# Kernel optimization log

Hardware: AMD Instinct MI355X
Metric: run time of the kernel (lower is better)

The kernel has to match this reference:

```python
import jax, jax.numpy as jnp
import numpy as np

N, E = 50000, 800000
IN_DIM, HID, OUT, HEADS = 128, 128, 64, 4
C1 = HID // HEADS  # 32 per-head channels in gat1
NEG_SLOPE = 0.2


def _gat_conv(x, src, dst, W, a_src, a_dst, b, heads, ch):
    """PyG GATConv (inference): gather -> edge attention -> segment softmax -> scatter."""
    n = x.shape[0]
    h = (x @ W).reshape(n, heads, ch)                      # [N,H,C]
    alpha_src = jnp.einsum('nhc,hc->nh', h, a_src)         # [N,H]
    alpha_dst = jnp.einsum('nhc,hc->nh', h, a_dst)         # [N,H]
    e = jax.nn.leaky_relu(alpha_src[src] + alpha_dst[dst], NEG_SLOPE)  # [E,H]
    m = jax.ops.segment_max(e, dst, num_segments=n)        # per-target max (stable softmax)
    e = jnp.exp(e - m[dst])
    denom = jax.ops.segment_sum(e, dst, num_segments=n)
    alpha = e / (denom[dst] + 1e-16)                       # [E,H]
    out = jax.ops.segment_sum(h[src] * alpha[:, :, None], dst, num_segments=n)  # [N,H,C]
    return out.reshape(n, heads * ch) + b


def setup_inputs() -> dict:
    key = jax.random.key(0)
    ks = jax.random.split(key, 16)
    x = jax.random.normal(ks[0], (N, IN_DIM), dtype=jnp.float32)
    edge_index = jax.random.randint(ks[1], (2, E), 0, N, dtype=jnp.int64)
    s = lambda fan_in: 1.0 / np.sqrt(fan_in)
    return {
        'x': x,
        'edge_index': edge_index,
        'W1': jax.random.normal(ks[2], (IN_DIM, HEADS * C1), jnp.float32) * s(IN_DIM),
        'a_src1': jax.random.normal(ks[3], (HEADS, C1), jnp.float32) * s(C1),
        'a_dst1': jax.random.normal(ks[4], (HEADS, C1), jnp.float32) * s(C1),
        'b1': jnp.zeros((HID,), jnp.float32),
        'W2': jax.random.normal(ks[5], (HID, OUT), jnp.float32) * s(HID),
        'a_src2': jax.random.normal(ks[6], (1, OUT), jnp.float32) * s(OUT),
        'a_dst2': jax.random.normal(ks[7], (1, OUT), jnp.float32) * s(OUT),
        'b2': jnp.zeros((OUT,), jnp.float32),
        'pw1': jax.random.normal(ks[8], (OUT, OUT), jnp.float32) * s(OUT),
        'pb1': jnp.zeros((OUT,), jnp.float32),
        'pw2': jax.random.normal(ks[9], (OUT, OUT), jnp.float32) * s(OUT),
        'pb2': jnp.zeros((OUT,), jnp.float32),
    }


def reference(x, edge_index, W1, a_src1, a_dst1, b1, W2, a_src2, a_dst2, b2, pw1, pb1, pw2, pb2):
    n = x.shape[0]
    # PyG GATConv add_self_loops=True
    loops = jnp.arange(n, dtype=edge_index.dtype)
    src = jnp.concatenate([edge_index[0], loops])
    dst = jnp.concatenate([edge_index[1], loops])
    h = jax.nn.elu(_gat_conv(x, src, dst, W1, a_src1, a_dst1, b1, HEADS, C1))
    h = jax.nn.elu(_gat_conv(h, src, dst, W2, a_src2, a_dst2, b2, 1, OUT))
    # origin_proj: Linear -> ReLU -> Linear
    h = jax.nn.relu(h @ pw1 + pb1)
    return h @ pw2 + pb2
```

## Files before the change

kernel.cpp:

```cpp
#include <hip/hip_runtime.h>
#include <math.h>

#define N_NODES 50000
#define N_EDGES 800000
#define ET (N_EDGES + N_NODES)
#define IN_DIM 128
#define HID 128
#define OUT_DIM 64
#define BW 64
#define NBUCK ((N_NODES + BW - 1) / BW)
#define NBLK 256
#define EPB 3328

typedef __attribute__((ext_vector_type(8))) short bf16x8;
typedef __attribute__((ext_vector_type(4))) float f32x4;

__device__ __forceinline__ float lrelu(float x){ return x >= 0.f ? x : 0.2f * x; }
__device__ __forceinline__ float eluf(float x){ return x > 0.f ? x : expm1f(x); }
__device__ __forceinline__ unsigned f2bf(float f){
    unsigned u = __float_as_uint(f);
    return (u + 0x7fffu + ((u >> 16) & 1u)) >> 16;
}
__device__ __forceinline__ float bflo(unsigned u){ return __uint_as_float(u << 16); }
__device__ __forceinline__ float bfhi(unsigned u){ return __uint_as_float(u & 0xffff0000u); }

__global__ __launch_bounds__(256) void k_count(const int* __restrict__ dst, int* __restrict__ C)
{
    __shared__ int cnt[NBUCK];
    const int tid = threadIdx.x, blk = blockIdx.x;
    for (int i = tid; i < NBUCK; i += 256) cnt[i] = 0;
    __syncthreads();
    #pragma unroll
    for (int j = 0; j < EPB / 256; j++) {
        const int e = blk * EPB + j * 256 + tid;
        if (e < ET) {
            const int d = (e < N_EDGES) ? dst[e] : (e - N_EDGES);
            atomicAdd(&cnt[d >> 6], 1);
        }
    }
    __syncthreads();
    for (int b = tid; b < NBUCK; b += 256) C[b * NBLK + blk] = cnt[b];
}

__global__ __launch_bounds__(256) void k_bsumA(const int* __restrict__ C, int* __restrict__ bsum2)
{
    __shared__ int red[4];
    int v = C[blockIdx.x * NBLK + threadIdx.x];
    #pragma unroll
    for (int off = 32; off > 0; off >>= 1) v += __shfl_down(v, off);
    if ((threadIdx.x & 63) == 0) red[threadIdx.x >> 6] = v;
    __syncthreads();
    if (threadIdx.x == 0) bsum2[blockIdx.x] = red[0] + red[1] + red[2] + red[3];
}

__global__ __launch_bounds__(1024) void k_bscanB(const int* __restrict__ bsum2, int* __restrict__ boff2)
{
    __shared__ int part[1024];
    const int t = threadIdx.x;
    int v = (t < NBUCK) ? bsum2[t] : 0;
    part[t] = v;
    __syncthreads();
    #pragma unroll
    for (int d = 1; d < 1024; d <<= 1) {
        int add = (t >= d) ? part[t - d] : 0;
        __syncthreads();
        part[t] += add;
        __syncthreads();
    }
    if (t < NBUCK) boff2[t] = part[t] - v;
    if (t == 0) boff2[NBUCK] = ET;
}

__global__ __launch_bounds__(256) void k_cscanC(const int* __restrict__ C,
                                                const int* __restrict__ boff2,
                                                int* __restrict__ Cs)
{
    __shared__ int part[256];
    const int t = threadIdx.x, b = blockIdx.x;
    int v = C[b * NBLK + t];
    part[t] = v;
    __syncthreads();
    #pragma unroll
    for (int d = 1; d < 256; d <<= 1) {
        int add = (t >= d) ? part[t - d] : 0;
        __syncthreads();
        part[t] += add;
        __syncthreads();
    }
    Cs[b * NBLK + t] = boff2[b] + part[t] - v;
}

__global__ __launch_bounds__(256) void k_part2(const int* __restrict__ src,
                                               const int* __restrict__ dst,
                                               const int* __restrict__ Cs,
                                               uint2* __restrict__ part)
{
    __shared__ int base[NBUCK];
    __shared__ int cnt[NBUCK];
    const int tid = threadIdx.x, blk = blockIdx.x;
    for (int b = tid; b < NBUCK; b += 256) { base[b] = Cs[b * NBLK + blk]; cnt[b] = 0; }
    __syncthreads();
    #pragma unroll
    for (int j = 0; j < EPB / 256; j++) {
        const int e = blk * EPB + j * 256 + tid;
        if (e < ET) {
            int s, d;
            if (e < N_EDGES) { s = src[e]; d = dst[e]; } else { s = d = e - N_EDGES; }
            const int b = d >> 6;
            const int r = atomicAdd(&cnt[b], 1);
            part[base[b] + r] = make_uint2((unsigned)d, (unsigned)s);
        }
    }
}

__global__ __launch_bounds__(256) void k_scat2(const int* __restrict__ boff2,
                                               const uint2* __restrict__ part,
                                               int* __restrict__ rowptr,
                                               int* __restrict__ csr_src)
{
    __shared__ int cnt64[BW];
    __shared__ int nbase[BW];
    const int b = blockIdx.x, tid = threadIdx.x;
    const int n0 = b * BW;
    const int lo = boff2[b], hi = boff2[b + 1];
    if (tid < BW) cnt64[tid] = 0;
    __syncthreads();
    for (int i = lo + tid; i < hi; i += 256) {
        atomicAdd(&cnt64[part[i].x & (BW - 1)], 1);
    }
    __syncthreads();
    if (tid < BW) {
        int v = cnt64[tid];
        int incl = v;
        #pragma unroll
        for (int off = 1; off < 64; off <<= 1) {
            int t2 = __shfl_up(incl, off);
            if (tid >= off) incl += t2;
        }
        const int excl = incl - v;
        nbase[tid] = excl;
        const int n = n0 + tid;
        if (n < N_NODES) rowptr[n] = lo + excl;
        cnt64[tid] = 0;
    }
    if (b == 0 && tid == 0) rowptr[N_NODES] = ET;
    __syncthreads();
    for (int i = lo + tid; i < hi; i += 256) {
        const uint2 p = part[i];
        const int dn = (int)p.x & (BW - 1);
        const int r = atomicAdd(&cnt64[dn], 1);
        csr_src[lo + nbase[dn] + r] = (int)p.y;
    }
}

__global__ __launch_bounds__(256, 2) void k_gemm1(
    const float* __restrict__ x, const float* __restrict__ W1,
    const float* __restrict__ a_s, const float* __restrict__ a_d,
    unsigned* __restrict__ h1b, float* __restrict__ as1, float* __restrict__ ad1)
{
    __shared__ unsigned sWt[128 * 68];
    __shared__ unsigned sxb[64 * 68];
    const int tid = threadIdx.x;
    const int wave = tid >> 6;
    const int lane = tid & 63;
    const int ll   = lane & 15;
    const int quad = lane >> 4;
    const int n0 = blockIdx.x * 64;

    for (int idx = tid; idx < 8192; idx += 256) {
        const int n = idx & 127, kp = idx >> 7;
        const float w0 = W1[(2 * kp) * 128 + n];
        const float w1 = W1[(2 * kp + 1) * 128 + n];
        sWt[n * 68 + kp] = f2bf(w0) | (f2bf(w1) << 16);
    }
    for (int idx = tid; idx < 4096; idx += 256) {
        const int node = idx >> 6, kp = idx & 63;
        const int n = n0 + node;
        unsigned pk = 0;
        if (n < N_NODES) {
            const float x0 = x[n * 128 + 2 * kp];
            const float x1 = x[n * 128 + 2 * kp + 1];
            pk = f2bf(x0) | (f2bf(x1) << 16);
        }
        sxb[node * 68 + kp] = pk;
    }
    __syncthreads();

    f32x4 acc[8];
    #pragma unroll
    for (int t = 0; t < 8; t++) acc[t] = (f32x4){0.f, 0.f, 0.f, 0.f};

    #pragma unroll
    for (int kk = 0; kk < 4; kk++) {
        const int kpo = 16 * kk + 4 * quad;
        const bf16x8 a = *(const bf16x8*)&sxb[(16 * wave + ll) * 68 + kpo];
        #pragma unroll
        for (int t = 0; t < 8; t++) {
            const bf16x8 b = *(const bf16x8*)&sWt[(16 * t + ll) * 68 + kpo];
            acc[t] = __builtin_amdgcn_mfma_f32_16x16x32_bf16(a, b, acc[t], 0, 0, 0);
        }
    }

    float as_v[8], ad_v[8];
    #pragma unroll
    for (int t = 0; t < 8; t++) { as_v[t] = a_s[16 * t + ll]; ad_v[t] = a_d[16 * t + ll]; }
    unsigned short* h1u = (unsigned short*)h1b;
    #pragma unroll
    for (int r = 0; r < 4; r++) {
        const int n = n0 + 16 * wave + 4 * quad + r;
        float ps0 = acc[0][r] * as_v[0] + acc[1][r] * as_v[1];
        float ps1 = acc[2][r] * as_v[2] + acc[3][r] * as_v[3];
        float ps2 = acc[4][r] * as_v[4] + acc[5][r] * as_v[5];
        float ps3 = acc[6][r] * as_v[6] + acc[7][r] * as_v[7];
        float pd0 = acc[0][r] * ad_v[0] + acc[1][r] * ad_v[1];
        float pd1 = acc[2][r] * ad_v[2] + acc[3][r] * ad_v[3];
        float pd2 = acc[4][r] * ad_v[4] + acc[5][r] * ad_v[5];
        float pd3 = acc[6][r] * ad_v[6] + acc[7][r] * ad_v[7];
        #pragma unroll
        for (int off = 1; off < 16; off <<= 1) {
            ps0 += __shfl_xor(ps0, off); ps1 += __shfl_xor(ps1, off);
            ps2 += __shfl_xor(ps2, off); ps3 += __shfl_xor(ps3, off);
            pd0 += __shfl_xor(pd0, off); pd1 += __shfl_xor(pd1, off);
            pd2 += __shfl_xor(pd2, off); pd3 += __shfl_xor(pd3, off);
        }
        if (n < N_NODES) {
            #pragma unroll
            for (int t = 0; t < 8; t++)
                h1u[n * 128 + 16 * t + ll] = (unsigned short)f2bf(acc[t][r]);
            if (ll == 0) {
                as1[n * 4 + 0] = ps0; as1[n * 4 + 1] = ps1;
                as1[n * 4 + 2] = ps2; as1[n * 4 + 3] = ps3;
                ad1[n * 4 + 0] = pd0; ad1[n * 4 + 1] = pd1;
                ad1[n * 4 + 2] = pd2; ad1[n * 4 + 3] = pd3;
            }
        }
    }
}

__global__ __launch_bounds__(256) void k_aggr1(
    const int* __restrict__ rowptr, const int* __restrict__ csr_src,
    const float* __restrict__ as1, const float* __restrict__ ad1,
    const uint4* __restrict__ h1u4, float* __restrict__ acc1)
{
    const int d  = blockIdx.x * 16 + (threadIdx.x >> 4);
    const int c8 = threadIdx.x & 15;
    const int hd = c8 >> 2;
    const int r0 = rowptr[d], r1 = rowptr[d + 1];
    const float adv = ad1[d * 4 + hd];
    float den = 0.f;
    float acc[8];
    #pragma unroll
    for (int m = 0; m < 8; m++) acc[m] = 0.f;
    int i = r0;
    for (; i + 2 <= r1; i += 2) {
        const int s0 = csr_src[i], s1 = csr_src[i + 1];
        const float e0 = as1[s0 * 4 + hd], e1 = as1[s1 * 4 + hd];
        const uint4 u0 = h1u4[s0 * 16 + c8];
        const uint4 u1 = h1u4[s1 * 16 + c8];
        const float w0 = expf(lrelu(e0 + adv));
        const float w1 = expf(lrelu(e1 + adv));
        den += w0 + w1;
        acc[0] = fmaf(bflo(u0.x), w0, acc[0]); acc[1] = fmaf(bfhi(u0.x), w0, acc[1]);
        acc[2] = fmaf(bflo(u0.y), w0, acc[2]); acc[3] = fmaf(bfhi(u0.y), w0, acc[3]);
        acc[4] = fmaf(bflo(u0.z), w0, acc[4]); acc[5] = fmaf(bfhi(u0.z), w0, acc[5]);
        acc[6] = fmaf(bflo(u0.w), w0, acc[6]); acc[7] = fmaf(bfhi(u0.w), w0, acc[7]);
        acc[0] = fmaf(bflo(u1.x), w1, acc[0]); acc[1] = fmaf(bfhi(u1.x), w1, acc[1]);
        acc[2] = fmaf(bflo(u1.y), w1, acc[2]); acc[3] = fmaf(bfhi(u1.y), w1, acc[3]);
        acc[4] = fmaf(bflo(u1.z), w1, acc[4]); acc[5] = fmaf(bfhi(u1.z), w1, acc[5]);
        acc[6] = fmaf(bflo(u1.w), w1, acc[6]); acc[7] = fmaf(bfhi(u1.w), w1, acc[7]);
    }
    if (i < r1) {
        const int s = csr_src[i];
        const float w = expf(lrelu(as1[s * 4 + hd] + adv));
        const uint4 u = h1u4[s * 16 + c8];
        den += w;
        acc[0] = fmaf(bflo(u.x), w, acc[0]); acc[1] = fmaf(bfhi(u.x), w, acc[1]);
        acc[2] = fmaf(bflo(u.y), w, acc[2]); acc[3] = fmaf(bfhi(u.y), w, acc[3]);
        acc[4] = fmaf(bflo(u.z), w, acc[4]); acc[5] = fmaf(bfhi(u.z), w, acc[5]);
        acc[6] = fmaf(bflo(u.w), w, acc[6]); acc[7] = fmaf(bfhi(u.w), w, acc[7]);
    }
    const float inv = 1.f / (den + 1e-16f);
    float4 o0 = make_float4(acc[0] * inv, acc[1] * inv, acc[2] * inv, acc[3] * inv);
    float4 o1 = make_float4(acc[4] * inv, acc[5] * inv, acc[6] * inv, acc[7] * inv);
    ((float4*)acc1)[d * 32 + 2 * c8 + 0] = o0;
    ((float4*)acc1)[d * 32 + 2 * c8 + 1] = o1;
}

__global__ __launch_bounds__(256, 4) void k_layer2(
    const float* __restrict__ acc1, const float* __restrict__ b1,
    const float* __restrict__ W2, const float* __restrict__ a_s2, const float* __restrict__ a_d2,
    unsigned* __restrict__ h2b, float* __restrict__ as2, float* __restrict__ ad2)
{
    __shared__ unsigned sWt[64 * 68];
    __shared__ unsigned sxb[64 * 68];
    const int tid = threadIdx.x;
    const int wave = tid >> 6;
    const int lane = tid & 63;
    const int ll   = lane & 15;
    const int quad = lane >> 4;
    const int n0 = blockIdx.x * 64;

    for (int idx = tid; idx < 4096; idx += 256) {
        const int n = idx & 63, kp = idx >> 6;
        const float w0 = W2[(2 * kp) * 64 + n];
        const float w1 = W2[(2 * kp + 1) * 64 + n];
        sWt[n * 68 + kp] = f2bf(w0) | (f2bf(w1) << 16);
    }
    for (int idx = tid; idx < 4096; idx += 256) {
        const int node = idx >> 6, kp = idx & 63;
        const int n = n0 + node;
        unsigned pk = 0;
        if (n < N_NODES) {
            const float v0 = eluf(acc1[n * 128 + 2 * kp]     + b1[2 * kp]);
            const float v1 = eluf(acc1[n * 128 + 2 * kp + 1] + b1[2 * kp + 1]);
            pk = f2bf(v0) | (f2bf(v1) << 16);
        }
        sxb[node * 68 + kp] = pk;
    }
    __syncthreads();

    f32x4 acc[4];
    #pragma unroll
    for (int t = 0; t < 4; t++) acc[t] = (f32x4){0.f, 0.f, 0.f, 0.f};

    #pragma unroll
    for (int kk = 0; kk < 4; kk++) {
        const int kpo = 16 * kk + 4 * quad;
        const bf16x8 a = *(const bf16x8*)&sxb[(16 * wave + ll) * 68 + kpo];
        #pragma unroll
        for (int t = 0; t < 4; t++) {
            const bf16x8 b = *(const bf16x8*)&sWt[(16 * t + ll) * 68 + kpo];
            acc[t] = __builtin_amdgcn_mfma_f32_16x16x32_bf16(a, b, acc[t], 0, 0, 0);
        }
    }

    float as_v[4], ad_v[4];
    #pragma unroll
    for (int t = 0; t < 4; t++) { as_v[t] = a_s2[16 * t + ll]; ad_v[t] = a_d2[16 * t + ll]; }
    unsigned short* h2u = (unsigned short*)h2b;
    #pragma unroll
    for (int r = 0; r < 4; r++) {
        const int n = n0 + 16 * wave + 4 * quad + r;
        float ps = acc[0][r] * as_v[0] + acc[1][r] * as_v[1]
                 + acc[2][r] * as_v[2] + acc[3][r] * as_v[3];
        float pd = acc[0][r] * ad_v[0] + acc[1][r] * ad_v[1]
                 + acc[2][r] * ad_v[2] + acc[3][r] * ad_v[3];
        #pragma unroll
        for (int off = 1; off < 16; off <<= 1) {
            ps += __shfl_xor(ps, off);
            pd += __shfl_xor(pd, off);
        }
        if (n < N_NODES) {
            #pragma unroll
            for (int t = 0; t < 4; t++)
                h2u[n * 64 + 16 * t + ll] = (unsigned short)f2bf(acc[t][r]);
            if (ll == 0) { as2[n] = ps; ad2[n] = pd; }
        }
    }
}

__global__ __launch_bounds__(256) void k_aggr2(
    const int* __restrict__ rowptr, const int* __restrict__ csr_src,
    const float* __restrict__ as2, const float* __restrict__ ad2,
    const uint4* __restrict__ h2u4, float* __restrict__ acc2)
{
    const int d  = blockIdx.x * 32 + (threadIdx.x >> 3);
    const int c8 = threadIdx.x & 7;
    if (d >= N_NODES) return;
    const int r0 = rowptr[d], r1 = rowptr[d + 1];
    const float adv = ad2[d];
    float den = 0.f;
    float acc[8];
    #pragma unroll
    for (int m = 0; m < 8; m++) acc[m] = 0.f;
    int i = r0;
    for (; i + 2 <= r1; i += 2) {
        const int s0 = csr_src[i], s1 = csr_src[i + 1];
        const float e0 = as2[s0], e1 = as2[s1];
        const uint4 u0 = h2u4[s0 * 8 + c8];
        const uint4 u1 = h2u4[s1 * 8 + c8];
        const float w0 = expf(lrelu(e0 + adv));
        const float w1 = expf(lrelu(e1 + adv));
        den += w0 + w1;
        acc[0] = fmaf(bflo(u0.x), w0, acc[0]); acc[1] = fmaf(bfhi(u0.x), w0, acc[1]);
        acc[2] = fmaf(bflo(u0.y), w0, acc[2]); acc[3] = fmaf(bfhi(u0.y), w0, acc[3]);
        acc[4] = fmaf(bflo(u0.z), w0, acc[4]); acc[5] = fmaf(bfhi(u0.z), w0, acc[5]);
        acc[6] = fmaf(bflo(u0.w), w0, acc[6]); acc[7] = fmaf(bfhi(u0.w), w0, acc[7]);
        acc[0] = fmaf(bflo(u1.x), w1, acc[0]); acc[1] = fmaf(bfhi(u1.x), w1, acc[1]);
        acc[2] = fmaf(bflo(u1.y), w1, acc[2]); acc[3] = fmaf(bfhi(u1.y), w1, acc[3]);
        acc[4] = fmaf(bflo(u1.z), w1, acc[4]); acc[5] = fmaf(bfhi(u1.z), w1, acc[5]);
        acc[6] = fmaf(bflo(u1.w), w1, acc[6]); acc[7] = fmaf(bfhi(u1.w), w1, acc[7]);
    }
    if (i < r1) {
        const int s = csr_src[i];
        const float w = expf(lrelu(as2[s] + adv));
        const uint4 u = h2u4[s * 8 + c8];
        den += w;
        acc[0] = fmaf(bflo(u.x), w, acc[0]); acc[1] = fmaf(bfhi(u.x), w, acc[1]);
        acc[2] = fmaf(bflo(u.y), w, acc[2]); acc[3] = fmaf(bfhi(u.y), w, acc[3]);
        acc[4] = fmaf(bflo(u.z), w, acc[4]); acc[5] = fmaf(bfhi(u.z), w, acc[5]);
        acc[6] = fmaf(bflo(u.w), w, acc[6]); acc[7] = fmaf(bfhi(u.w), w, acc[7]);
    }
    const float inv = 1.f / (den + 1e-16f);
    float4 o0 = make_float4(acc[0] * inv, acc[1] * inv, acc[2] * inv, acc[3] * inv);
    float4 o1 = make_float4(acc[4] * inv, acc[5] * inv, acc[6] * inv, acc[7] * inv);
    ((float4*)acc2)[d * 16 + 2 * c8 + 0] = o0;
    ((float4*)acc2)[d * 16 + 2 * c8 + 1] = o1;
}

__global__ __launch_bounds__(256, 2) void k_out(
    const float* __restrict__ acc2, const float* __restrict__ b2,
    const float* __restrict__ pw1, const float* __restrict__ pb1,
    const float* __restrict__ pw2, const float* __restrict__ pb2,
    float* __restrict__ out)
{
    __shared__ float s1[64 * 64];
    __shared__ float s2[64 * 64];
    __shared__ float so[64][68];
    __shared__ float sp[64][68];
    const int tid = threadIdx.x;
    for (int i = tid; i < 1024; i += 256) {
        ((float4*)s1)[i] = ((const float4*)pw1)[i];
        ((float4*)s2)[i] = ((const float4*)pw2)[i];
    }
    const int cg = tid & 15;
    const int ng = tid >> 4;
    const float4 pb1_4 = ((const float4*)pb1)[cg];
    const float4 pb2_4 = ((const float4*)pb2)[cg];
    const int nGroups = (N_NODES + 63) / 64;
    for (int g = blockIdx.x; g < nGroups; g += gridDim.x) {
        const int n0 = g * 64;
        __syncthreads();
        #pragma unroll
        for (int j = 0; j < 4; j++) {
            const int i = tid + 256 * j;
            const int node = i >> 4, quad = i & 15;
            const int n = n0 + node;
            float4 v = make_float4(0.f, 0.f, 0.f, 0.f);
            if (n < N_NODES) {
                v = ((const float4*)acc2)[n * 16 + quad];
                const float4 bb = ((const float4*)b2)[quad];
                v.x = eluf(v.x + bb.x);
                v.y = eluf(v.y + bb.y);
                v.z = eluf(v.z + bb.z);
                v.w = eluf(v.w + bb.w);
            }
            *(float4*)&so[node][4 * quad] = v;
        }
        __syncthreads();
        float4 p[4];
        #pragma unroll
        for (int m = 0; m < 4; m++) p[m] = pb1_4;
        #pragma unroll 8
        for (int k = 0; k < 64; k++) {
            const float4 w = *(const float4*)&s1[k * 64 + 4 * cg];
            #pragma unroll
            for (int m = 0; m < 4; m++) {
                const float xv = so[4 * ng + m][k];
                p[m].x = fmaf(xv, w.x, p[m].x);
                p[m].y = fmaf(xv, w.y, p[m].y);
                p[m].z = fmaf(xv, w.z, p[m].z);
                p[m].w = fmaf(xv, w.w, p[m].w);
            }
        }
        #pragma unroll
        for (int m = 0; m < 4; m++) {
            p[m].x = fmaxf(p[m].x, 0.f); p[m].y = fmaxf(p[m].y, 0.f);
            p[m].z = fmaxf(p[m].z, 0.f); p[m].w = fmaxf(p[m].w, 0.f);
            *(float4*)&sp[4 * ng + m][4 * cg] = p[m];
        }
        __syncthreads();
        float4 o[4];
        #pragma unroll
        for (int m = 0; m < 4; m++) o[m] = pb2_4;
        #pragma unroll 8
        for (int k = 0; k < 64; k++) {
            const float4 w = *(const float4*)&s2[k * 64 + 4 * cg];
            #pragma unroll
            for (int m = 0; m < 4; m++) {
                const float xv = sp[4 * ng + m][k];
                o[m].x = fmaf(xv, w.x, o[m].x);
                o[m].y = fmaf(xv, w.y, o[m].y);
                o[m].z = fmaf(xv, w.z, o[m].z);
                o[m].w = fmaf(xv, w.w, o[m].w);
            }
        }
        #pragma unroll
        for (int m = 0; m < 4; m++) {
            const int n = n0 + 4 * ng + m;
            if (n < N_NODES) ((float4*)out)[n * 16 + cg] = o[m];
        }
    }
}

extern "C" void kernel_launch(void* const* d_in, const int* in_sizes, int n_in,
                              void* d_out, int out_size, void* d_ws, size_t ws_size,
                              hipStream_t stream)
{
    const float* x      = (const float*)d_in[0];
    const int*   ei     = (const int*)d_in[1];
    const int*   src    = ei;
    const int*   dst    = ei + N_EDGES;
    const float* W1     = (const float*)d_in[2];
    const float* a_src1 = (const float*)d_in[3];
    const float* a_dst1 = (const float*)d_in[4];
    const float* b1     = (const float*)d_in[5];
    const float* W2     = (const float*)d_in[6];
    const float* a_src2 = (const float*)d_in[7];
    const float* a_dst2 = (const float*)d_in[8];
    const float* b2     = (const float*)d_in[9];
    const float* pw1    = (const float*)d_in[10];
    const float* pb1    = (const float*)d_in[11];
    const float* pw2    = (const float*)d_in[12];
    const float* pb2    = (const float*)d_in[13];

    uint2* part  = (uint2*)d_ws;
    int* ibase   = (int*)(part + ET);
    int* rowptr  = ibase;
    int* C       = rowptr + 50001;
    int* Cs      = C + 200192;
    int* bsum2   = Cs + 200192;
    int* boff2   = bsum2 + 782;
    int* csr_src = boff2 + 785;
    unsigned* h1b = (unsigned*)(csr_src + 850000);
    unsigned* h2b = h1b + 3200000;
    float* fws   = (float*)(h2b + 1600000);
    float* as1   = fws;
    float* ad1   = as1 + 200000;
    float* acc1  = ad1 + 200000;
    float* as2   = acc1 + 6400000;
    float* ad2   = as2 + 50000;
    float* acc2  = ad2 + 50000;

    k_count<<<NBLK, 256, 0, stream>>>(dst, C);
    k_bsumA<<<NBUCK, 256, 0, stream>>>(C, bsum2);
    k_bscanB<<<1, 1024, 0, stream>>>(bsum2, boff2);
    k_cscanC<<<NBUCK, 256, 0, stream>>>(C, boff2, Cs);
    k_part2<<<NBLK, 256, 0, stream>>>(src, dst, Cs, part);
    k_scat2<<<NBUCK, 256, 0, stream>>>(boff2, part, rowptr, csr_src);

    k_gemm1<<<(N_NODES + 63) / 64, 256, 0, stream>>>(x, W1, a_src1, a_dst1, h1b, as1, ad1);
    k_aggr1<<<N_NODES / 16, 256, 0, stream>>>(rowptr, csr_src, as1, ad1,
                                              (const uint4*)h1b, acc1);

    k_layer2<<<(N_NODES + 63) / 64, 256, 0, stream>>>(acc1, b1, W2, a_src2, a_dst2, h2b, as2, ad2);
    k_aggr2<<<(N_NODES + 31) / 32, 256, 0, stream>>>(rowptr, csr_src, as2, ad2,
                                                     (const uint4*)h2b, acc2);

    k_out<<<782, 256, 0, stream>>>(acc2, b2, pw1, pb1, pw2, pb2, (float*)d_out);
}
```

Before: 249.0 us.

## Fuse gemm1 with partition, fold bias+ELU into aggr1, merge aggr2 with output MLP

Merges the layer-1 GEMM and the edge partition kernel into one launch with block-index dispatch so the two independent jobs run concurrently. Layer-1 aggregation now applies bias and ELU and writes bf16 directly, so layer 2 loads half as much data and the fp32 intermediate goes away. Layer-2 aggregation is fused with the two-layer output MLP in a 512-thread kernel, removing the acc2 round trip. Both aggregation loops are unrolled by four to keep more gathers in flight, at the cost of more register pressure.

```diff
diff --git a/kernel.cpp b/kernel.cpp
--- a/kernel.cpp
+++ b/kernel.cpp
@@ -11,6 +11,7 @@
 #define NBUCK ((N_NODES + BW - 1) / BW)
 #define NBLK 256
 #define EPB 3328
+#define NT64 ((N_NODES + 63) / 64)
 
 typedef __attribute__((ext_vector_type(8))) short bf16x8;
 typedef __attribute__((ext_vector_type(4))) float f32x4;
@@ -90,25 +91,109 @@
     Cs[b * NBLK + t] = boff2[b] + part[t] - v;
 }
 
-__global__ __launch_bounds__(256) void k_part2(const int* __restrict__ src,
-                                               const int* __restrict__ dst,
-                                               const int* __restrict__ Cs,
-                                               uint2* __restrict__ part)
-{
-    __shared__ int base[NBUCK];
-    __shared__ int cnt[NBUCK];
-    const int tid = threadIdx.x, blk = blockIdx.x;
-    for (int b = tid; b < NBUCK; b += 256) { base[b] = Cs[b * NBLK + blk]; cnt[b] = 0; }
-    __syncthreads();
-    #pragma unroll
-    for (int j = 0; j < EPB / 256; j++) {
-        const int e = blk * EPB + j * 256 + tid;
-        if (e < ET) {
-            int s, d;
-            if (e < N_EDGES) { s = src[e]; d = dst[e]; } else { s = d = e - N_EDGES; }
-            const int b = d >> 6;
-            const int r = atomicAdd(&cnt[b], 1);
-            part[base[b] + r] = make_uint2((unsigned)d, (unsigned)s);
+__global__ __launch_bounds__(256, 2) void k_gemm1_part2(
+    const float* __restrict__ x, const float* __restrict__ W1,
+    const float* __restrict__ a_s, const float* __restrict__ a_d,
+    unsigned* __restrict__ h1b, float* __restrict__ as1, float* __restrict__ ad1,
+    const int* __restrict__ src, const int* __restrict__ dst,
+    const int* __restrict__ Cs, uint2* __restrict__ part)
+{
+    __shared__ unsigned smem[128 * 68 + 64 * 68];
+    const int tid = threadIdx.x;
+
+    if (blockIdx.x < NT64) {
+        unsigned* sWt = smem;
+        unsigned* sxb = smem + 128 * 68;
+        const int wave = tid >> 6;
+        const int lane = tid & 63;
+        const int ll   = lane & 15;
+        const int quad = lane >> 4;
+        const int n0 = blockIdx.x * 64;
+
+        for (int idx = tid; idx < 8192; idx += 256) {
+            const int n = idx & 127, kp = idx >> 7;
+            const float w0 = W1[(2 * kp) * 128 + n];
+            const float w1 = W1[(2 * kp + 1) * 128 + n];
+            sWt[n * 68 + kp] = f2bf(w0) | (f2bf(w1) << 16);
+        }
+        for (int idx = tid; idx < 4096; idx += 256) {
+            const int node = idx >> 6, kp = idx & 63;
+            const int n = n0 + node;
+            unsigned pk = 0;
+            if (n < N_NODES) {
+                const float x0 = x[n * 128 + 2 * kp];
+                const float x1 = x[n * 128 + 2 * kp + 1];
+                pk = f2bf(x0) | (f2bf(x1) << 16);
+            }
+            sxb[node * 68 + kp] = pk;
+        }
+        __syncthreads();
+
+        f32x4 acc[8];
+        #pragma unroll
+        for (int t = 0; t < 8; t++) acc[t] = (f32x4){0.f, 0.f, 0.f, 0.f};
+
+        #pragma unroll
+        for (int kk = 0; kk < 4; kk++) {
+            const int kpo = 16 * kk + 4 * quad;
+            const bf16x8 a = *(const bf16x8*)&sxb[(16 * wave + ll) * 68 + kpo];
+            #pragma unroll
+            for (int t = 0; t < 8; t++) {
+                const bf16x8 b = *(const bf16x8*)&sWt[(16 * t + ll) * 68 + kpo];
+                acc[t] = __builtin_amdgcn_mfma_f32_16x16x32_bf16(a, b, acc[t], 0, 0, 0);
+            }
+        }
+
+        float as_v[8], ad_v[8];
+        #pragma unroll
+        for (int t = 0; t < 8; t++) { as_v[t] = a_s[16 * t + ll]; ad_v[t] = a_d[16 * t + ll]; }
+        unsigned short* h1u = (unsigned short*)h1b;
+        #pragma unroll
+        for (int r = 0; r < 4; r++) {
+            const int n = n0 + 16 * wave + 4 * quad + r;
+            float ps0 = acc[0][r] * as_v[0] + acc[1][r] * as_v[1];
+            float ps1 = acc[2][r] * as_v[2] + acc[3][r] * as_v[3];
+            float ps2 = acc[4][r] * as_v[4] + acc[5][r] * as_v[5];
+            float ps3 = acc[6][r] * as_v[6] + acc[7][r] * as_v[7];
+            float pd0 = acc[0][r] * ad_v[0] + acc[1][r] * ad_v[1];
+            float pd1 = acc[2][r] * ad_v[2] + acc[3][r] * ad_v[3];
+            float pd2 = acc[4][r] * ad_v[4] + acc[5][r] * ad_v[5];
+            float pd3 = acc[6][r] * ad_v[6] + acc[7][r] * ad_v[7];
+            #pragma unroll
+            for (int off = 1; off < 16; off <<= 1) {
+                ps0 += __shfl_xor(ps0, off); ps1 += __shfl_xor(ps1, off);
+                ps2 += __shfl_xor(ps2, off); ps3 += __shfl_xor(ps3, off);
+                pd0 += __shfl_xor(pd0, off); pd1 += __shfl_xor(pd1, off);
+                pd2 += __shfl_xor(pd2, off); pd3 += __shfl_xor(pd3, off);
+            }
+            if (n < N_NODES) {
+                #pragma unroll
+                for (int t = 0; t < 8; t++)
+                    h1u[n * 128 + 16 * t + ll] = (unsigned short)f2bf(acc[t][r]);
+                if (ll == 0) {
+                    as1[n * 4 + 0] = ps0; as1[n * 4 + 1] = ps1;
+                    as1[n * 4 + 2] = ps2; as1[n * 4 + 3] = ps3;
+                    ad1[n * 4 + 0] = pd0; ad1[n * 4 + 1] = pd1;
+                    ad1[n * 4 + 2] = pd2; ad1[n * 4 + 3] = pd3;
+                }
+            }
+        }
+    } else {
+        const int blk = blockIdx.x - NT64;
+        int* base = (int*)smem;
+        int* cnt  = (int*)smem + NBUCK;
+        for (int b = tid; b < NBUCK; b += 256) { base[b] = Cs[b * NBLK + blk]; cnt[b] = 0; }
+        __syncthreads();
+        #pragma unroll
+        for (int j = 0; j < EPB / 256; j++) {
+            const int e = blk * EPB + j * 256 + tid;
+            if (e < ET) {
+                int s, d;
+                if (e < N_EDGES) { s = src[e]; d = dst[e]; } else { s = d = e - N_EDGES; }
+                const int b = d >> 6;
+                const int r = atomicAdd(&cnt[b], 1);
+                part[base[b] + r] = make_uint2((unsigned)d, (unsigned)s);
+            }
         }
     }
 }
@@ -153,94 +238,11 @@
     }
 }
 
-__global__ __launch_bounds__(256, 2) void k_gemm1(
-    const float* __restrict__ x, const float* __restrict__ W1,
-    const float* __restrict__ a_s, const float* __restrict__ a_d,
-    unsigned* __restrict__ h1b, float* __restrict__ as1, float* __restrict__ ad1)
-{
-    __shared__ unsigned sWt[128 * 68];
-    __shared__ unsigned sxb[64 * 68];
-    const int tid = threadIdx.x;
-    const int wave = tid >> 6;
-    const int lane = tid & 63;
-    const int ll   = lane & 15;
-    const int quad = lane >> 4;
-    const int n0 = blockIdx.x * 64;
-
-    for (int idx = tid; idx < 8192; idx += 256) {
-        const int n = idx & 127, kp = idx >> 7;
-        const float w0 = W1[(2 * kp) * 128 + n];
-        const float w1 = W1[(2 * kp + 1) * 128 + n];
-        sWt[n * 68 + kp] = f2bf(w0) | (f2bf(w1) << 16);
-    }
-    for (int idx = tid; idx < 4096; idx += 256) {
-        const int node = idx >> 6, kp = idx & 63;
-        const int n = n0 + node;
-        unsigned pk = 0;
-        if (n < N_NODES) {
-            const float x0 = x[n * 128 + 2 * kp];
-            const float x1 = x[n * 128 + 2 * kp + 1];
-            pk = f2bf(x0) | (f2bf(x1) << 16);
-        }
-        sxb[node * 68 + kp] = pk;
-    }
-    __syncthreads();
-
-    f32x4 acc[8];
-    #pragma unroll
-    for (int t = 0; t < 8; t++) acc[t] = (f32x4){0.f, 0.f, 0.f, 0.f};
-
-    #pragma unroll
-    for (int kk = 0; kk < 4; kk++) {
-        const int kpo = 16 * kk + 4 * quad;
-        const bf16x8 a = *(const bf16x8*)&sxb[(16 * wave + ll) * 68 + kpo];
-        #pragma unroll
-        for (int t = 0; t < 8; t++) {
-            const bf16x8 b = *(const bf16x8*)&sWt[(16 * t + ll) * 68 + kpo];
-            acc[t] = __builtin_amdgcn_mfma_f32_16x16x32_bf16(a, b, acc[t], 0, 0, 0);
-        }
-    }
-
-    float as_v[8], ad_v[8];
-    #pragma unroll
-    for (int t = 0; t < 8; t++) { as_v[t] = a_s[16 * t + ll]; ad_v[t] = a_d[16 * t + ll]; }
-    unsigned short* h1u = (unsigned short*)h1b;
-    #pragma unroll
-    for (int r = 0; r < 4; r++) {
-        const int n = n0 + 16 * wave + 4 * quad + r;
-        float ps0 = acc[0][r] * as_v[0] + acc[1][r] * as_v[1];
-        float ps1 = acc[2][r] * as_v[2] + acc[3][r] * as_v[3];
-        float ps2 = acc[4][r] * as_v[4] + acc[5][r] * as_v[5];
-        float ps3 = acc[6][r] * as_v[6] + acc[7][r] * as_v[7];
-        float pd0 = acc[0][r] * ad_v[0] + acc[1][r] * ad_v[1];
-        float pd1 = acc[2][r] * ad_v[2] + acc[3][r] * ad_v[3];
-        float pd2 = acc[4][r] * ad_v[4] + acc[5][r] * ad_v[5];
-        float pd3 = acc[6][r] * ad_v[6] + acc[7][r] * ad_v[7];
-        #pragma unroll
-        for (int off = 1; off < 16; off <<= 1) {
-            ps0 += __shfl_xor(ps0, off); ps1 += __shfl_xor(ps1, off);
-            ps2 += __shfl_xor(ps2, off); ps3 += __shfl_xor(ps3, off);
-            pd0 += __shfl_xor(pd0, off); pd1 += __shfl_xor(pd1, off);
-            pd2 += __shfl_xor(pd2, off); pd3 += __shfl_xor(pd3, off);
-        }
-        if (n < N_NODES) {
-            #pragma unroll
-            for (int t = 0; t < 8; t++)
-                h1u[n * 128 + 16 * t + ll] = (unsigned short)f2bf(acc[t][r]);
-            if (ll == 0) {
-                as1[n * 4 + 0] = ps0; as1[n * 4 + 1] = ps1;
-                as1[n * 4 + 2] = ps2; as1[n * 4 + 3] = ps3;
-                ad1[n * 4 + 0] = pd0; ad1[n * 4 + 1] = pd1;
-                ad1[n * 4 + 2] = pd2; ad1[n * 4 + 3] = pd3;
-            }
-        }
-    }
-}
-
 __global__ __launch_bounds__(256) void k_aggr1(
     const int* __restrict__ rowptr, const int* __restrict__ csr_src,
     const float* __restrict__ as1, const float* __restrict__ ad1,
-    const uint4* __restrict__ h1u4, float* __restrict__ acc1)
+    const uint4* __restrict__ h1u4, const float* __restrict__ b1,
+    unsigned* __restrict__ hEb)
 {
     const int d  = blockIdx.x * 16 + (threadIdx.x >> 4);
     const int c8 = threadIdx.x & 15;
@@ -252,14 +254,20 @@
     #pragma unroll
     for (int m = 0; m < 8; m++) acc[m] = 0.f;
     int i = r0;
-    for (; i + 2 <= r1; i += 2) {
-        const int s0 = csr_src[i], s1 = csr_src[i + 1];
+    for (; i + 4 <= r1; i += 4) {
+        const int s0 = csr_src[i],     s1 = csr_src[i + 1];
+        const int s2 = csr_src[i + 2], s3 = csr_src[i + 3];
         const float e0 = as1[s0 * 4 + hd], e1 = as1[s1 * 4 + hd];
+        const float e2 = as1[s2 * 4 + hd], e3 = as1[s3 * 4 + hd];
         const uint4 u0 = h1u4[s0 * 16 + c8];
         const uint4 u1 = h1u4[s1 * 16 + c8];
+        const uint4 u2 = h1u4[s2 * 16 + c8];
+        const uint4 u3 = h1u4[s3 * 16 + c8];
         const float w0 = expf(lrelu(e0 + adv));
         const float w1 = expf(lrelu(e1 + adv));
-        den += w0 + w1;
+        const float w2 = expf(lrelu(e2 + adv));
+        const float w3 = expf(lrelu(e3 + adv));
+        den += (w0 + w1) + (w2 + w3);
         acc[0] = fmaf(bflo(u0.x), w0, acc[0]); acc[1] = fmaf(bfhi(u0.x), w0, acc[1]);
         acc[2] = fmaf(bflo(u0.y), w0, acc[2]); acc[3] = fmaf(bfhi(u0.y), w0, acc[3]);
         acc[4] = fmaf(bflo(u0.z), w0, acc[4]); acc[5] = fmaf(bfhi(u0.z), w0, acc[5]);
@@ -268,8 +276,16 @@
         acc[2] = fmaf(bflo(u1.y), w1, acc[2]); acc[3] = fmaf(bfhi(u1.y), w1, acc[3]);
         acc[4] = fmaf(bflo(u1.z), w1, acc[4]); acc[5] = fmaf(bfhi(u1.z), w1, acc[5]);
         acc[6] = fmaf(bflo(u1.w), w1, acc[6]); acc[7] = fmaf(bfhi(u1.w), w1, acc[7]);
-    }
-    if (i < r1) {
+        acc[0] = fmaf(bflo(u2.x), w2, acc[0]); acc[1] = fmaf(bfhi(u2.x), w2, acc[1]);
+        acc[2] = fmaf(bflo(u2.y), w2, acc[2]); acc[3] = fmaf(bfhi(u2.y), w2, acc[3]);
+        acc[4] = fmaf(bflo(u2.z), w2, acc[4]); acc[5] = fmaf(bfhi(u2.z), w2, acc[5]);
+        acc[6] = fmaf(bflo(u2.w), w2, acc[6]); acc[7] = fmaf(bfhi(u2.w), w2, acc[7]);
+        acc[0] = fmaf(bflo(u3.x), w3, acc[0]); acc[1] = fmaf(bfhi(u3.x), w3, acc[1]);
+        acc[2] = fmaf(bflo(u3.y), w3, acc[2]); acc[3] = fmaf(bfhi(u3.y), w3, acc[3]);
+        acc[4] = fmaf(bflo(u3.z), w3, acc[4]); acc[5] = fmaf(bfhi(u3.z), w3, acc[5]);
+        acc[6] = fmaf(bflo(u3.w), w3, acc[6]); acc[7] = fmaf(bfhi(u3.w), w3, acc[7]);
+    }
+    for (; i < r1; ++i) {
         const int s = csr_src[i];
         const float w = expf(lrelu(as1[s * 4 + hd] + adv));
         const uint4 u = h1u4[s * 16 + c8];
@@ -280,14 +296,26 @@
         acc[6] = fmaf(bflo(u.w), w, acc[6]); acc[7] = fmaf(bfhi(u.w), w, acc[7]);
     }
     const float inv = 1.f / (den + 1e-16f);
-    float4 o0 = make_float4(acc[0] * inv, acc[1] * inv, acc[2] * inv, acc[3] * inv);
-    float4 o1 = make_float4(acc[4] * inv, acc[5] * inv, acc[6] * inv, acc[7] * inv);
-    ((float4*)acc1)[d * 32 + 2 * c8 + 0] = o0;
-    ((float4*)acc1)[d * 32 + 2 * c8 + 1] = o1;
+    const float4 bA = ((const float4*)b1)[2 * c8];
+    const float4 bB = ((const float4*)b1)[2 * c8 + 1];
+    const float v0 = eluf(acc[0] * inv + bA.x);
+    const float v1 = eluf(acc[1] * inv + bA.y);
+    const float v2 = eluf(acc[2] * inv + bA.z);
+    const float v3 = eluf(acc[3] * inv + bA.w);
+    const float v4 = eluf(acc[4] * inv + bB.x);
+    const float v5 = eluf(acc[5] * inv + bB.y);
+    const float v6 = eluf(acc[6] * inv + bB.z);
+    const float v7 = eluf(acc[7] * inv + bB.w);
+    uint4 o;
+    o.x = f2bf(v0) | (f2bf(v1) << 16);
+    o.y = f2bf(v2) | (f2bf(v3) << 16);
+    o.z = f2bf(v4) | (f2bf(v5) << 16);
+    o.w = f2bf(v6) | (f2bf(v7) << 16);
+    ((uint4*)hEb)[d * 16 + c8] = o;
 }
 
 __global__ __launch_bounds__(256, 4) void k_layer2(
-    const float* __restrict__ acc1, const float* __restrict__ b1,
+    const unsigned* __restrict__ hEb,
     const float* __restrict__ W2, const float* __restrict__ a_s2, const float* __restrict__ a_d2,
     unsigned* __restrict__ h2b, float* __restrict__ as2, float* __restrict__ ad2)
 {
@@ -306,16 +334,14 @@
         const float w1 = W2[(2 * kp + 1) * 64 + n];
         sWt[n * 68 + kp] = f2bf(w0) | (f2bf(w1) << 16);
     }
-    for (int idx = tid; idx < 4096; idx += 256) {
-        const int node = idx >> 6, kp = idx & 63;
+    const uint4* hE4 = (const uint4*)hEb;
+    for (int idx = tid; idx < 1024; idx += 256) {
+        const int node = idx >> 4, q = idx & 15;
         const int n = n0 + node;
-        unsigned pk = 0;
-        if (n < N_NODES) {
-            const float v0 = eluf(acc1[n * 128 + 2 * kp]     + b1[2 * kp]);
-            const float v1 = eluf(acc1[n * 128 + 2 * kp + 1] + b1[2 * kp + 1]);
-            pk = f2bf(v0) | (f2bf(v1) << 16);
-        }
-        sxb[node * 68 + kp] = pk;
+        uint4 pk = make_uint4(0, 0, 0, 0);
+        if (n < N_NODES) pk = hE4[n * 16 + q];
+        unsigned* dstp = &sxb[node * 68 + 4 * q];
+        dstp[0] = pk.x; dstp[1] = pk.y; dstp[2] = pk.z; dstp[3] = pk.w;
     }
     __syncthreads();
 
@@ -359,57 +385,10 @@
     }
 }
 
-__global__ __launch_bounds__(256) void k_aggr2(
+__global__ __launch_bounds__(512, 4) void k_tail(
     const int* __restrict__ rowptr, const int* __restrict__ csr_src,
     const float* __restrict__ as2, const float* __restrict__ ad2,
-    const uint4* __restrict__ h2u4, float* __restrict__ acc2)
-{
-    const int d  = blockIdx.x * 32 + (threadIdx.x >> 3);
-    const int c8 = threadIdx.x & 7;
-    if (d >= N_NODES) return;
-    const int r0 = rowptr[d], r1 = rowptr[d + 1];
-    const float adv = ad2[d];
-    float den = 0.f;
-    float acc[8];
-    #pragma unroll
-    for (int m = 0; m < 8; m++) acc[m] = 0.f;
-    int i = r0;
-    for (; i + 2 <= r1; i += 2) {
-        const int s0 = csr_src[i], s1 = csr_src[i + 1];
-        const float e0 = as2[s0], e1 = as2[s1];
-        const uint4 u0 = h2u4[s0 * 8 + c8];
-        const uint4 u1 = h2u4[s1 * 8 + c8];
-        const float w0 = expf(lrelu(e0 + adv));
-        const float w1 = expf(lrelu(e1 + adv));
-        den += w0 + w1;
-        acc[0] = fmaf(bflo(u0.x), w0, acc[0]); acc[1] = fmaf(bfhi(u0.x), w0, acc[1]);
-        acc[2] = fmaf(bflo(u0.y), w0, acc[2]); acc[3] = fmaf(bfhi(u0.y), w0, acc[3]);
-        acc[4] = fmaf(bflo(u0.z), w0, acc[4]); acc[5] = fmaf(bfhi(u0.z), w0, acc[5]);
-        acc[6] = fmaf(bflo(u0.w), w0, acc[6]); acc[7] = fmaf(bfhi(u0.w), w0, acc[7]);
-        acc[0] = fmaf(bflo(u1.x), w1, acc[0]); acc[1] = fmaf(bfhi(u1.x), w1, acc[1]);
-        acc[2] = fmaf(bflo(u1.y), w1, acc[2]); acc[3] = fmaf(bfhi(u1.y), w1, acc[3]);
-        acc[4] = fmaf(bflo(u1.z), w1, acc[4]); acc[5] = fmaf(bfhi(u1.z), w1, acc[5]);
-        acc[6] = fmaf(bflo(u1.w), w1, acc[6]); acc[7] = fmaf(bfhi(u1.w), w1, acc[7]);
-    }
-    if (i < r1) {
-        const int s = csr_src[i];
-        const float w = expf(lrelu(as2[s] + adv));
-        const uint4 u = h2u4[s * 8 + c8];
-        den += w;
-        acc[0] = fmaf(bflo(u.x), w, acc[0]); acc[1] = fmaf(bfhi(u.x), w, acc[1]);
-        acc[2] = fmaf(bflo(u.y), w, acc[2]); acc[3] = fmaf(bfhi(u.y), w, acc[3]);
-        acc[4] = fmaf(bflo(u.z), w, acc[4]); acc[5] = fmaf(bfhi(u.z), w, acc[5]);
-        acc[6] = fmaf(bflo(u.w), w, acc[6]); acc[7] = fmaf(bfhi(u.w), w, acc[7]);
-    }
-    const float inv = 1.f / (den + 1e-16f);
-    float4 o0 = make_float4(acc[0] * inv, acc[1] * inv, acc[2] * inv, acc[3] * inv);
-    float4 o1 = make_float4(acc[4] * inv, acc[5] * inv, acc[6] * inv, acc[7] * inv);
-    ((float4*)acc2)[d * 16 + 2 * c8 + 0] = o0;
-    ((float4*)acc2)[d * 16 + 2 * c8 + 1] = o1;
-}
-
-__global__ __launch_bounds__(256, 2) void k_out(
-    const float* __restrict__ acc2, const float* __restrict__ b2,
+    const uint4* __restrict__ h2u4, const float* __restrict__ b2,
     const float* __restrict__ pw1, const float* __restrict__ pb1,
     const float* __restrict__ pw2, const float* __restrict__ pb2,
     float* __restrict__ out)
@@ -419,77 +398,129 @@
     __shared__ float so[64][68];
     __shared__ float sp[64][68];
     const int tid = threadIdx.x;
-    for (int i = tid; i < 1024; i += 256) {
+    const int n0 = blockIdx.x * 64;
+
+    for (int i = tid; i < 1024; i += 512) {
         ((float4*)s1)[i] = ((const float4*)pw1)[i];
         ((float4*)s2)[i] = ((const float4*)pw2)[i];
     }
+
+    {
+        const int dl = tid >> 3;
+        const int c8 = tid & 7;
+        const int d = n0 + dl;
+        float acc[8];
+        #pragma unroll
+        for (int m = 0; m < 8; m++) acc[m] = 0.f;
+        float v0 = 0.f, v1 = 0.f, v2 = 0.f, v3 = 0.f;
+        float v4 = 0.f, v5 = 0.f, v6 = 0.f, v7 = 0.f;
+        if (d < N_NODES) {
+            const int r0 = rowptr[d], r1 = rowptr[d + 1];
+            const float adv = ad2[d];
+            float den = 0.f;
+            int i = r0;
+            for (; i + 4 <= r1; i += 4) {
+                const int s0 = csr_src[i],     s1_ = csr_src[i + 1];
+                const int s2_ = csr_src[i + 2], s3_ = csr_src[i + 3];
+                const float e0 = as2[s0], e1 = as2[s1_], e2 = as2[s2_], e3 = as2[s3_];
+                const uint4 u0 = h2u4[s0  * 8 + c8];
+                const uint4 u1 = h2u4[s1_ * 8 + c8];
+                const uint4 u2 = h2u4[s2_ * 8 + c8];
+                const uint4 u3 = h2u4[s3_ * 8 + c8];
+                const float w0 = expf(lrelu(e0 + adv));
+                const float w1 = expf(lrelu(e1 + adv));
+                const float w2 = expf(lrelu(e2 + adv));
+                const float w3 = expf(lrelu(e3 + adv));
+                den += (w0 + w1) + (w2 + w3);
+                acc[0] = fmaf(bflo(u0.x), w0, acc[0]); acc[1] = fmaf(bfhi(u0.x), w0, acc[1]);
+                acc[2] = fmaf(bflo(u0.y), w0, acc[2]); acc[3] = fmaf(bfhi(u0.y), w0, acc[3]);
+                acc[4] = fmaf(bflo(u0.z), w0, acc[4]); acc[5] = fmaf(bfhi(u0.z), w0, acc[5]);
+                acc[6] = fmaf(bflo(u0.w), w0, acc[6]); acc[7] = fmaf(bfhi(u0.w), w0, acc[7]);
+                acc[0] = fmaf(bflo(u1.x), w1, acc[0]); acc[1] = fmaf(bfhi(u1.x), w1, acc[1]);
+                acc[2] = fmaf(bflo(u1.y), w1, acc[2]); acc[3] = fmaf(bfhi(u1.y), w1, acc[3]);
+                acc[4] = fmaf(bflo(u1.z), w1, acc[4]); acc[5] = fmaf(bfhi(u1.z), w1, acc[5]);
+                acc[6] = fmaf(bflo(u1.w), w1, acc[6]); acc[7] = fmaf(bfhi(u1.w), w1, acc[7]);
+                acc[0] = fmaf(bflo(u2.x), w2, acc[0]); acc[1] = fmaf(bfhi(u2.x), w2, acc[1]);
+                acc[2] = fmaf(bflo(u2.y), w2, acc[2]); acc[3] = fmaf(bfhi(u2.y), w2, acc[3]);
+                acc[4] = fmaf(bflo(u2.z), w2, acc[4]); acc[5] = fmaf(bfhi(u2.z), w2, acc[5]);
+                acc[6] = fmaf(bflo(u2.w), w2, acc[6]); acc[7] = fmaf(bfhi(u2.w), w2, acc[7]);
+                acc[0] = fmaf(bflo(u3.x), w3, acc[0]); acc[1] = fmaf(bfhi(u3.x), w3, acc[1]);
+                acc[2] = fmaf(bflo(u3.y), w3, acc[2]); acc[3] = fmaf(bfhi(u3.y), w3, acc[3]);
+                acc[4] = fmaf(bflo(u3.z), w3, acc[4]); acc[5] = fmaf(bfhi(u3.z), w3, acc[5]);
+                acc[6] = fmaf(bflo(u3.w), w3, acc[6]); acc[7] = fmaf(bfhi(u3.w), w3, acc[7]);
+            }
+            for (; i < r1; ++i) {
+                const int s = csr_src[i];
+                const float w = expf(lrelu(as2[s] + adv));
+                const uint4 u = h2u4[s * 8 + c8];
+                den += w;
+                acc[0] = fmaf(bflo(u.x), w, acc[0]); acc[1] = fmaf(bfhi(u.x), w, acc[1]);
+                acc[2] = fmaf(bflo(u.y), w, acc[2]); acc[3] = fmaf(bfhi(u.y), w, acc[3]);
+                acc[4] = fmaf(bflo(u.z), w, acc[4]); acc[5] = fmaf(bfhi(u.z), w, acc[5]);
+                acc[6] = fmaf(bflo(u.w), w, acc[6]); acc[7] = fmaf(bfhi(u.w), w, acc[7]);
+            }
+            const float inv = 1.f / (den + 1e-16f);
+            const float4 bA = ((const float4*)b2)[2 * c8];
+            const float4 bB = ((const float4*)b2)[2 * c8 + 1];
+            v0 = eluf(acc[0] * inv + bA.x);
+            v1 = eluf(acc[1] * inv + bA.y);
+            v2 = eluf(acc[2] * inv + bA.z);
+            v3 = eluf(acc[3] * inv + bA.w);
+            v4 = eluf(acc[4] * inv + bB.x);
+            v5 = eluf(acc[5] * inv + bB.y);
+            v6 = eluf(acc[6] * inv + bB.z);
+            v7 = eluf(acc[7] * inv + bB.w);
+        }
+        *(float4*)&so[dl][8 * c8]     = make_float4(v0, v1, v2, v3);
+        *(float4*)&so[dl][8 * c8 + 4] = make_float4(v4, v5, v6, v7);
+    }
+    __syncthreads();
+
     const int cg = tid & 15;
     const int ng = tid >> 4;
     const float4 pb1_4 = ((const float4*)pb1)[cg];
     const float4 pb2_4 = ((const float4*)pb2)[cg];
-    const int nGroups = (N_NODES + 63) / 64;
-    for (int g = blockIdx.x; g < nGroups; g += gridDim.x) {
-        const int n0 = g * 64;
-        __syncthreads();
-        #pragma unroll
-        for (int j = 0; j < 4; j++) {
-            const int i = tid + 256 * j;
-            const int node = i >> 4, quad = i & 15;
-            const int n = n0 + node;
-            float4 v = make_float4(0.f, 0.f, 0.f, 0.f);
-            if (n < N_NODES) {
-                v = ((const float4*)acc2)[n * 16 + quad];
-                const float4 bb = ((const float4*)b2)[quad];
-                v.x = eluf(v.x + bb.x);
-                v.y = eluf(v.y + bb.y);
-                v.z = eluf(v.z + bb.z);
-                v.w = eluf(v.w + bb.w);
-            }
-            *(float4*)&so[node][4 * quad] = v;
-        }
-        __syncthreads();
-        float4 p[4];
-        #pragma unroll
-        for (int m = 0; m < 4; m++) p[m] = pb1_4;
-        #pragma unroll 8
-        for (int k = 0; k < 64; k++) {
-            const float4 w = *(const float4*)&s1[k * 64 + 4 * cg];
-            #pragma unroll
-            for (int m = 0; m < 4; m++) {
-                const float xv = so[4 * ng + m][k];
-                p[m].x = fmaf(xv, w.x, p[m].x);
-                p[m].y = fmaf(xv, w.y, p[m].y);
-                p[m].z = fmaf(xv, w.z, p[m].z);
-                p[m].w = fmaf(xv, w.w, p[m].w);
-            }
-        }
-        #pragma unroll
-        for (int m = 0; m < 4; m++) {
-            p[m].x = fmaxf(p[m].x, 0.f); p[m].y = fmaxf(p[m].y, 0.f);
-            p[m].z = fmaxf(p[m].z, 0.f); p[m].w = fmaxf(p[m].w, 0.f);
-            *(float4*)&sp[4 * ng + m][4 * cg] = p[m];
-        }
-        __syncthreads();
-        float4 o[4];
-        #pragma unroll
-        for (int m = 0; m < 4; m++) o[m] = pb2_4;
-        #pragma unroll 8
-        for (int k = 0; k < 64; k++) {
-            const float4 w = *(const float4*)&s2[k * 64 + 4 * cg];
-            #pragma unroll
-            for (int m = 0; m < 4; m++) {
-                const float xv = sp[4 * ng + m][k];
-                o[m].x = fmaf(xv, w.x, o[m].x);
-                o[m].y = fmaf(xv, w.y, o[m].y);
-                o[m].z = fmaf(xv, w.z, o[m].z);
-                o[m].w = fmaf(xv, w.w, o[m].w);
-            }
-        }
-        #pragma unroll
-        for (int m = 0; m < 4; m++) {
-            const int n = n0 + 4 * ng + m;
-            if (n < N_NODES) ((float4*)out)[n * 16 + cg] = o[m];
-        }
+    float4 p[2];
+    #pragma unroll
+    for (int m = 0; m < 2; m++) p[m] = pb1_4;
+    #pragma unroll 8
+    for (int k = 0; k < 64; k++) {
+        const float4 w = *(const float4*)&s1[k * 64 + 4 * cg];
+        #pragma unroll
+        for (int m = 0; m < 2; m++) {
+            const float xv = so[2 * ng + m][k];
+            p[m].x = fmaf(xv, w.x, p[m].x);
+            p[m].y = fmaf(xv, w.y, p[m].y);
+            p[m].z = fmaf(xv, w.z, p[m].z);
+            p[m].w = fmaf(xv, w.w, p[m].w);
+        }
+    }
+    #pragma unroll
+    for (int m = 0; m < 2; m++) {
+        p[m].x = fmaxf(p[m].x, 0.f); p[m].y = fmaxf(p[m].y, 0.f);
+        p[m].z = fmaxf(p[m].z, 0.f); p[m].w = fmaxf(p[m].w, 0.f);
+        *(float4*)&sp[2 * ng + m][4 * cg] = p[m];
+    }
+    __syncthreads();
+    float4 o[2];
+    #pragma unroll
+    for (int m = 0; m < 2; m++) o[m] = pb2_4;
+    #pragma unroll 8
+    for (int k = 0; k < 64; k++) {
+        const float4 w = *(const float4*)&s2[k * 64 + 4 * cg];
+        #pragma unroll
+        for (int m = 0; m < 2; m++) {
+            const float xv = sp[2 * ng + m][k];
+            o[m].x = fmaf(xv, w.x, o[m].x);
+            o[m].y = fmaf(xv, w.y, o[m].y);
+            o[m].z = fmaf(xv, w.z, o[m].z);
+            o[m].w = fmaf(xv, w.w, o[m].w);
+        }
+    }
+    #pragma unroll
+    for (int m = 0; m < 2; m++) {
+        const int n = n0 + 2 * ng + m;
+        if (n < N_NODES) ((float4*)out)[n * 16 + cg] = o[m];
     }
 }
 
@@ -527,25 +558,26 @@
     float* fws   = (float*)(h2b + 1600000);
     float* as1   = fws;
     float* ad1   = as1 + 200000;
-    float* acc1  = ad1 + 200000;
-    float* as2   = acc1 + 6400000;
+    unsigned* hEb = (unsigned*)(ad1 + 200000);
+    float* as2   = (float*)(hEb + 3200000);
     float* ad2   = as2 + 50000;
-    float* acc2  = ad2 + 50000;
 
     k_count<<<NBLK, 256, 0, stream>>>(dst, C);
     k_bsumA<<<NBUCK, 256, 0, stream>>>(C, bsum2);
     k_bscanB<<<1, 1024, 0, stream>>>(bsum2, boff2);
     k_cscanC<<<NBUCK, 256, 0, stream>>>(C, boff2, Cs);
-    k_part2<<<NBLK, 256, 0, stream>>>(src, dst, Cs, part);
+
+    k_gemm1_part2<<<NT64 + NBLK, 256, 0, stream>>>(x, W1, a_src1, a_dst1,
+                                                   h1b, as1, ad1,
+                                                   src, dst, Cs, part);
     k_scat2<<<NBUCK, 256, 0, stream>>>(boff2, part, rowptr, csr_src);
 
-    k_gemm1<<<(N_NODES + 63) / 64, 256, 0, stream>>>(x, W1, a_src1, a_dst1, h1b, as1, ad1);
     k_aggr1<<<N_NODES / 16, 256, 0, stream>>>(rowptr, csr_src, as1, ad1,
-                                              (const uint4*)h1b, acc1);
-
-    k_layer2<<<(N_NODES + 63) / 64, 256, 0, stream>>>(acc1, b1, W2, a_src2, a_dst2, h2b, as2, ad2);
-    k_aggr2<<<(N_NODES + 31) / 32, 256, 0, stream>>>(rowptr, csr_src, as2, ad2,
-                                                     (const uint4*)h2b, acc2);
-
-    k_out<<<782, 256, 0, stream>>>(acc2, b2, pw1, pb1, pw2, pb2, (float*)d_out);
-}
+                                              (const uint4*)h1b, b1, hEb);
+
+    k_layer2<<<NT64, 256, 0, stream>>>(hEb, W2, a_src2, a_dst2, h2b, as2, ad2);
+
+    k_tail<<<NT64, 512, 0, stream>>>(rowptr, csr_src, as2, ad2,
+                                     (const uint4*)h2b, b2,
+                                     pw1, pb1, pw2, pb2, (float*)d_out);
+}
```

Measured after the change: 224.1 us. 1.11x faster.
